# Optimization experiments

Measured on AMD Instinct MI355X. Metric: run time of the kernel, lower is better.

Reference implementation:

```python
import jax, jax.numpy as jnp
import numpy as np

D_MODEL = 1024
INNER = 2048      # expand=2
D_STATE = 16
D_CONV = 4
DT_RANK = 64      # ceil(1024/16)
DT_MIN, DT_MAX = 0.001, 0.1
RMS_EPS = 1e-6


def _causal_depthwise_conv1d(x, kernel, bias):
    # x: (B, L, C), kernel: (K, C)
    channels = x.shape[-1]
    rhs = kernel[:, None, :]  # (K, 1, C)
    out = jax.lax.conv_general_dilated(
        lhs=x, rhs=rhs, window_strides=(1,),
        padding=[(kernel.shape[0] - 1, 0)],
        dimension_numbers=("NWC", "WIO", "NWC"),
        feature_group_count=channels)
    return out + bias[None, None, :]


def _selective_scan(u, dt, b, c, a, d):
    # u, dt: (B, L, Di); b, c: (B, L, S); a: (Di, S); d: (Di,)
    da = jnp.exp(dt[..., None] * a)                  # (B, L, Di, S)
    db = (dt * u)[..., None] * b[:, :, None, :]      # (B, L, Di, S)

    def step(h, inp):
        da_t, db_t, c_t = inp
        h = da_t * h + db_t                          # (B, Di, S)
        y = jnp.einsum("bds,bs->bd", h, c_t)
        return h, y

    h0 = jnp.zeros((u.shape[0], u.shape[2], a.shape[1]), u.dtype)
    _, ys = jax.lax.scan(
        step, h0,
        (da.transpose(1, 0, 2, 3), db.transpose(1, 0, 2, 3), c.transpose(1, 0, 2)))
    return ys.transpose(1, 0, 2) + u * d             # (B, L, Di)


def setup_inputs() -> dict:
    key = jax.random.key(0)
    ks = jax.random.split(key, 16)

    def lin(k, fan_in, shape):
        return jax.random.normal(k, shape, jnp.float32) / np.sqrt(fan_in)

    a_init = jnp.log(jnp.arange(1, D_STATE + 1, dtype=jnp.float32))
    return {
        "x": jax.random.normal(ks[0], (2, 2048, D_MODEL), jnp.float32),
        "norm_scale": jnp.ones((D_MODEL,), jnp.float32),
        "in_proj_w": lin(ks[1], D_MODEL, (D_MODEL, 2 * INNER)),
        "in_proj_b": jnp.zeros((2 * INNER,), jnp.float32),
        "out_proj_w": lin(ks[2], INNER, (INNER, D_MODEL)),
        "out_proj_b": jnp.zeros((D_MODEL,), jnp.float32),
        "dt_in_w": lin(ks[3], INNER, (INNER, DT_RANK)),
        "dt_in_b": jnp.zeros((DT_RANK,), jnp.float32),
        "dt_out_w": lin(ks[4], DT_RANK, (DT_RANK, INNER)),
        "dt_out_b": jnp.zeros((INNER,), jnp.float32),
        "b_proj_w": lin(ks[5], INNER, (INNER, D_STATE)),
        "b_proj_b": jnp.zeros((D_STATE,), jnp.float32),
        "c_proj_w": lin(ks[6], INNER, (INNER, D_STATE)),
        "c_proj_b": jnp.zeros((D_STATE,), jnp.float32),
        "conv_kernel": jax.random.normal(ks[7], (D_CONV, INNER), jnp.float32) / np.sqrt(D_CONV),
        "conv_bias": jnp.zeros((INNER,), jnp.float32),
        "a_log": jnp.tile(a_init[None, :], (INNER, 1)),
        "d": jnp.ones((INNER,), jnp.float32),
        "dt_bias": jnp.zeros((INNER,), jnp.float32),
    }


def reference(x, norm_scale, in_proj_w, in_proj_b, out_proj_w, out_proj_b,
              dt_in_w, dt_in_b, dt_out_w, dt_out_b, b_proj_w, b_proj_b,
              c_proj_w, c_proj_b, conv_kernel, conv_bias, a_log, d, dt_bias):
    residual = x
    # RMSNorm
    var = jnp.mean(jnp.square(x), axis=-1, keepdims=True)
    xn = x * jax.lax.rsqrt(var + RMS_EPS) * norm_scale
    # in projection -> u, z
    uz = xn @ in_proj_w + in_proj_b
    u, z = jnp.split(uz, 2, axis=-1)
    # causal depthwise conv + silu
    u = _causal_depthwise_conv1d(u, conv_kernel, conv_bias)
    u = jax.nn.silu(u)
    # dt path (low-rank) -> softplus -> clip
    dt = (u @ dt_in_w + dt_in_b) @ dt_out_w + dt_out_b + dt_bias
    dt = jnp.clip(jax.nn.softplus(dt), DT_MIN, DT_MAX)
    # B, C projections with tanh
    b = jnp.tanh(u @ b_proj_w + b_proj_b)
    c = jnp.tanh(u @ c_proj_w + c_proj_b)
    # selective scan
    a = -jnp.exp(a_log)
    y = _selective_scan(u, dt, b, c, a, d)
    # gate, out projection, residual
    y = y * jax.nn.silu(z)
    y = y @ out_proj_w + out_proj_b
    return residual + y
```

## Files before the change

### kernel.cpp

```cpp
#include <hip/hip_runtime.h>
#include <cstdint>
#include <cstddef>

typedef unsigned short u16;
typedef __bf16 bf16x8 __attribute__((ext_vector_type(8)));
typedef float f32x4 __attribute__((ext_vector_type(4)));
typedef u16 u16x4 __attribute__((ext_vector_type(4)));

#define DMODEL 1024
#define DINNER 2048
#define NBATCH 2
#define LSEQ   2048
#define NTOK   4096
#define NSTATE 16
#define NCH    64
#define TCH    32

__device__ __forceinline__ u16 f2b(float f) {
  union { float f; unsigned u; } a; a.f = f;
  unsigned r = a.u + 0x7fffu + ((a.u >> 16) & 1u);
  return (u16)(r >> 16);
}
__device__ __forceinline__ float b2f(u16 h) {
  union { unsigned u; float f; } a; a.u = ((unsigned)h) << 16;
  return a.f;
}

__device__ __forceinline__ void gload_lds16(const u16* g, __bf16* l) {
  __builtin_amdgcn_global_load_lds(
      (const __attribute__((address_space(1))) unsigned int*)g,
      (__attribute__((address_space(3))) unsigned int*)l, 16, 0, 0);
}

__global__ __launch_bounds__(256)
void prep_all(const float* __restrict__ w_in, const float* __restrict__ w_out,
              const float* __restrict__ w_dti, const float* __restrict__ w_b,
              const float* __restrict__ w_c, const float* __restrict__ w_dto,
              const float* __restrict__ b_dto, const float* __restrict__ dtbias,
              const float* __restrict__ x, const float* __restrict__ nscale,
              u16* __restrict__ WINT, u16* __restrict__ WOUTT, u16* __restrict__ WBC,
              u16* __restrict__ WDT2T, float* __restrict__ DTB2, u16* __restrict__ XN) {
  __shared__ float sh[32 * 33];
  const int tid = threadIdx.x;
  const int xx = tid & 31, y0 = tid >> 5;
  int blk = blockIdx.x;
  if (blk < 4096) {
    int c0 = (blk & 127) * 32, r0 = (blk >> 7) * 32;
    #pragma unroll
    for (int yy = y0; yy < 32; yy += 8) sh[yy * 33 + xx] = w_in[(size_t)(r0 + yy) * 4096 + c0 + xx];
    __syncthreads();
    #pragma unroll
    for (int yy = y0; yy < 32; yy += 8) WINT[(size_t)(c0 + yy) * 1024 + r0 + xx] = f2b(sh[xx * 33 + yy]);
    return;
  }
  blk -= 4096;
  if (blk < 2048) {
    int c0 = (blk & 31) * 32, r0 = (blk >> 5) * 32;
    #pragma unroll
    for (int yy = y0; yy < 32; yy += 8) sh[yy * 33 + xx] = w_out[(size_t)(r0 + yy) * 1024 + c0 + xx];
    __syncthreads();
    #pragma unroll
    for (int yy = y0; yy < 32; yy += 8) WOUTT[(size_t)(c0 + yy) * 2048 + r0 + xx] = f2b(sh[xx * 33 + yy]);
    return;
  }
  blk -= 2048;
  if (blk < 192) {
    int c0 = (blk % 3) * 32, r0 = (blk / 3) * 32;
    #pragma unroll
    for (int yy = y0; yy < 32; yy += 8) {
      int r = r0 + yy, c = c0 + xx;
      float v = (c < 64) ? w_dti[(size_t)r * 64 + c]
                         : (c < 80 ? w_b[(size_t)r * 16 + (c - 64)] : w_c[(size_t)r * 16 + (c - 80)]);
      sh[yy * 33 + xx] = v;
    }
    __syncthreads();
    #pragma unroll
    for (int yy = y0; yy < 32; yy += 8) WBC[(size_t)(c0 + yy) * 2048 + r0 + xx] = f2b(sh[xx * 33 + yy]);
    return;
  }
  blk -= 192;
  if (blk < 128) {
    int c0 = (blk & 63) * 32, r0 = (blk >> 6) * 32;
    #pragma unroll
    for (int yy = y0; yy < 32; yy += 8) sh[yy * 33 + xx] = w_dto[(size_t)(r0 + yy) * 2048 + c0 + xx];
    __syncthreads();
    #pragma unroll
    for (int yy = y0; yy < 32; yy += 8) WDT2T[(size_t)(c0 + yy) * 64 + r0 + xx] = f2b(sh[xx * 33 + yy]);
    return;
  }
  blk -= 128;
  if (blk < 8) {
    int i = blk * 256 + tid;
    DTB2[i] = b_dto[i] + dtbias[i];
    return;
  }
  blk -= 8;
  {
    const float4* xp = (const float4*)(x + (size_t)blk * DMODEL);
    float4 v = xp[tid];
    float ss = v.x * v.x + v.y * v.y + v.z * v.z + v.w * v.w;
    #pragma unroll
    for (int o = 32; o; o >>= 1) ss += __shfl_down(ss, o);
    if ((tid & 63) == 0) sh[tid >> 6] = ss;
    __syncthreads();
    float tot = sh[0] + sh[1] + sh[2] + sh[3];
    float r = rsqrtf(tot * (1.0f / DMODEL) + 1e-6f);
    float4 sc = ((const float4*)nscale)[tid];
    u16x4 o4;
    o4[0] = f2b(v.x * r * sc.x); o4[1] = f2b(v.y * r * sc.y);
    o4[2] = f2b(v.z * r * sc.z); o4[3] = f2b(v.w * r * sc.w);
    *(u16x4*)(XN + (size_t)blk * DMODEL + tid * 4) = o4;
  }
}

template <int BM, int BN, int NWM, int NWN, int EPI>
__global__ __launch_bounds__(NWM * NWN * 64, 1)
void gemm_db(const u16* __restrict__ A, const u16* __restrict__ Bt,
             const float* __restrict__ bias, const float* __restrict__ res,
             void* __restrict__ outv, int M, int N, int K, int RM, int RN) {
  constexpr int NTHR = NWM * NWN * 64;
  constexpr int WMW = BM / NWM;
  constexpr int WNW = BN / NWN;
  constexpr int MF = WMW / 16;
  constexpr int NF = WNW / 16;
  constexpr int LPT = (BM + BN) * 8 / NTHR;
  __shared__ __bf16 lds[2][(BM + BN) * 64];
  const int tid = threadIdx.x;
  const int lane = tid & 63;
  const int wave = tid >> 6;
  const int wr = wave / NWN, wc = wave % NWN;

  const int GM = M / BM;
  const int bid = blockIdx.x;
  const int xcd = bid & 7;
  const int l = bid >> 3;
  const int rgm = GM / RM;
  const int rr = xcd % rgm, rc = xcd / rgm;
  const size_t m0 = (size_t)(rr * RM + (l % RM)) * BM;
  const size_t n0 = (size_t)(rc * RN + (l / RM)) * BN;
  const int NT = K >> 6;

#define STAGE_DB(bufi, k0)                                                     \
  { _Pragma("unroll")                                                          \
    for (int ss = 0; ss < BM * 8 / NTHR; ss++) {                               \
      int g = tid + ss * NTHR;                                                 \
      int row = g >> 3;                                                        \
      int kk = ((g & 7) * 8) ^ ((row & 7) << 3);                               \
      gload_lds16(A + (m0 + row) * K + (k0) + kk, &lds[bufi][g * 8]);          \
    }                                                                          \
    _Pragma("unroll")                                                          \
    for (int ss = 0; ss < BN * 8 / NTHR; ss++) {                               \
      int g = tid + ss * NTHR;                                                 \
      int row = g >> 3;                                                        \
      int kk = ((g & 7) * 8) ^ ((row & 7) << 3);                               \
      gload_lds16(Bt + (n0 + row) * K + (k0) + kk,                             \
                  &lds[bufi][BM * 64 + g * 8]);                                \
    } }

  f32x4 acc[MF][NF] = {};
  STAGE_DB(0, 0)
  STAGE_DB(1, 64)

  const int rsw = (lane & 7) << 3;
  const int arow0 = wr * WMW + (lane & 15);
  const int brow0 = wc * WNW + (lane & 15);
  const int kgrp = (lane >> 4) * 8;

  for (int t = 0; t < NT; t++) {
    const int cur = t & 1;
    if (t == NT - 1) asm volatile("s_waitcnt vmcnt(0)" ::: "memory");
    else             asm volatile("s_waitcnt vmcnt(%0)" :: "n"(LPT) : "memory");
    __builtin_amdgcn_s_barrier();
    asm volatile("" ::: "memory");
    const __bf16* As_ = &lds[cur][0];
    const __bf16* Bs_ = &lds[cur][BM * 64];
    #pragma unroll
    for (int qr = 0; qr < MF / 4; qr++) {
      #pragma unroll
      for (int qc = 0; qc < NF / 2; qc++) {
        bf16x8 af[2][4], bfv[2][2];
        #pragma unroll
        for (int ks = 0; ks < 2; ks++) {
          const int kk = (ks * 32 + kgrp) ^ rsw;
          #pragma unroll
          for (int i = 0; i < 4; i++)
            af[ks][i] = *(const bf16x8*)(As_ + (size_t)(arow0 + (qr * 4 + i) * 16) * 64 + kk);
          #pragma unroll
          for (int j = 0; j < 2; j++)
            bfv[ks][j] = *(const bf16x8*)(Bs_ + (size_t)(brow0 + (qc * 2 + j) * 16) * 64 + kk);
        }
        __builtin_amdgcn_s_setprio(1);
        #pragma unroll
        for (int ks = 0; ks < 2; ks++)
          #pragma unroll
          for (int i = 0; i < 4; i++)
            #pragma unroll
            for (int j = 0; j < 2; j++)
              acc[qr * 4 + i][qc * 2 + j] = __builtin_amdgcn_mfma_f32_16x16x32_bf16(
                  af[ks][i], bfv[ks][j], acc[qr * 4 + i][qc * 2 + j], 0, 0, 0);
        __builtin_amdgcn_s_setprio(0);
        __builtin_amdgcn_sched_barrier(0);
      }
    }
    __builtin_amdgcn_s_barrier();
    asm volatile("" ::: "memory");
    if (t + 2 < NT) { STAGE_DB(cur, (t + 2) * 64) }
  }

  const int cr = (lane >> 4) << 2;
  const int cc = lane & 15;
  #pragma unroll
  for (int fr = 0; fr < MF; fr++) {
    #pragma unroll
    for (int fc = 0; fc < NF; fc++) {
      const size_t col = n0 + wc * WNW + fc * 16 + cc;
      const float bv = bias[col];
      #pragma unroll
      for (int r = 0; r < 4; r++) {
        const size_t row = m0 + wr * WMW + fr * 16 + cr + r;
        if constexpr (EPI == 0) {
          ((u16*)outv)[row * N + col] = f2b(acc[fr][fc][r] + bv);
        } else {
          ((float*)outv)[row * N + col] = acc[fr][fc][r] + bv + res[row * N + col];
        }
      }
    }
  }
#undef STAGE_DB
}

template <int EPI, int BN>
__global__ __launch_bounds__(256)
void gemm_bt(const u16* __restrict__ A, const u16* __restrict__ Bt,
             const float* __restrict__ bias, const float* __restrict__ res,
             void* __restrict__ outv, int M, int N, int K, int ksplit) {
  constexpr int WN = BN / 2;
  constexpr int JN = WN / 16;
  __shared__ __bf16 As[128][72];
  __shared__ __bf16 Bs[BN][72];
  const int tid = threadIdx.x;
  const int m0 = blockIdx.y * 128;
  const int n0 = blockIdx.x * BN;
  const int wave = tid >> 6, lane = tid & 63;
  const int wm = (wave >> 1) * 64, wn = (wave & 1) * WN;
  const int sr = tid >> 3;
  const int sc = (tid & 7) * 8;
  const int kbeg = blockIdx.z * ksplit, kend = kbeg + ksplit;
  f32x4 acc[4][JN] = {};
  for (int k0 = kbeg; k0 < kend; k0 += 64) {
    __syncthreads();
    #pragma unroll
    for (int r = 0; r < 128; r += 32)
      *(bf16x8*)&As[sr + r][sc] = *(const bf16x8*)(A + (size_t)(m0 + sr + r) * K + k0 + sc);
    #pragma unroll
    for (int r = 0; r < BN; r += 32)
      *(bf16x8*)&Bs[sr + r][sc] = *(const bf16x8*)(Bt + (size_t)(n0 + sr + r) * K + k0 + sc);
    __syncthreads();
    #pragma unroll
    for (int ks = 0; ks < 64; ks += 32) {
      const int kr = ks + ((lane >> 4) << 3);
      bf16x8 af[4], bfr[JN];
      #pragma unroll
      for (int i = 0; i < 4; i++) af[i]  = *(const bf16x8*)&As[wm + (lane & 15) + i * 16][kr];
      #pragma unroll
      for (int j = 0; j < JN; j++) bfr[j] = *(const bf16x8*)&Bs[wn + (lane & 15) + j * 16][kr];
      #pragma unroll
      for (int i = 0; i < 4; i++)
        #pragma unroll
        for (int j = 0; j < JN; j++)
          acc[i][j] = __builtin_amdgcn_mfma_f32_16x16x32_bf16(af[i], bfr[j], acc[i][j], 0, 0, 0);
    }
  }
  const int cr = (lane >> 4) << 2;
  const int cc = lane & 15;
  #pragma unroll
  for (int i = 0; i < 4; i++) {
    #pragma unroll
    for (int j = 0; j < JN; j++) {
      const int col = n0 + wn + j * 16 + cc;
      #pragma unroll
      for (int r = 0; r < 4; r++) {
        const int row = m0 + wm + i * 16 + cr + r;
        float v = acc[i][j][r];
        if constexpr (EPI == 1) {
          ((float*)outv)[(size_t)blockIdx.z * M * N + (size_t)row * N + col] = v;
        } else {
          v += bias[col];
          v = (v > 20.0f) ? v : log1pf(__expf(v));
          v = fminf(fmaxf(v, 0.001f), 0.1f);
          ((u16*)outv)[(size_t)row * N + col] = f2b(v);
        }
      }
    }
  }
}

__global__ __launch_bounds__(256)
void conv_silu_seq(const u16* __restrict__ uz, const float* __restrict__ ck,
                   const float* __restrict__ cb, u16* __restrict__ u) {
  int d  = (blockIdx.x & 7) * 256 + threadIdx.x;
  int lc = (blockIdx.x >> 3) & 127;
  int b  = blockIdx.x >> 10;
  const float w0 = ck[d], w1 = ck[DINNER + d], w2 = ck[2 * DINNER + d], w3 = ck[3 * DINNER + d];
  const float bias = cb[d];
  const int t0 = lc * 16;
  float x0 = 0.f, x1 = 0.f, x2 = 0.f;
  #pragma unroll
  for (int j = -3; j < 0; j++) {
    int t = t0 + j;
    float v = (t >= 0) ? b2f(uz[((size_t)(b * LSEQ + t)) * (2 * DINNER) + d]) : 0.f;
    x0 = x1; x1 = x2; x2 = v;
  }
  #pragma unroll
  for (int i = 0; i < 16; i++) {
    int t = t0 + i;
    float x3 = b2f(uz[((size_t)(b * LSEQ + t)) * (2 * DINNER) + d]);
    float acc = bias + w0 * x0 + w1 * x1 + w2 * x2 + w3 * x3;
    float sv = acc / (1.0f + __expf(-acc));
    u[((size_t)(b * LSEQ + t)) * DINNER + d] = f2b(sv);
    x0 = x1; x1 = x2; x2 = x3;
  }
}

__global__ __launch_bounds__(256)
void prep_dtbc(const float* __restrict__ dtbc, const float* __restrict__ dtin_b,
               const float* __restrict__ bb, const float* __restrict__ cbias,
               u16* __restrict__ dt1, float* __restrict__ Bm, float* __restrict__ Cm) {
  int idx = blockIdx.x * 256 + threadIdx.x;
  if (idx >= NTOK * 96) return;
  int row = idx / 96, col = idx - row * 96;
  float v = 0.f;
  #pragma unroll
  for (int z = 0; z < 8; z++)
    v += dtbc[(size_t)z * NTOK * 96 + (size_t)row * 96 + col];
  if (col < 64)       dt1[(size_t)row * 64 + col] = f2b(v + dtin_b[col]);
  else if (col < 80)  Bm[(size_t)row * NSTATE + col - 64] = tanhf(v + bb[col - 64]);
  else                Cm[(size_t)row * NSTATE + col - 80] = tanhf(v + cbias[col - 80]);
}

__global__ __launch_bounds__(256)
void scan_pass1(const u16* __restrict__ dt, const u16* __restrict__ u,
                const float* __restrict__ Bm, const float* __restrict__ alog,
                float* __restrict__ chP, float* __restrict__ chS) {
  const int d  = (blockIdx.x & 7) * 256 + threadIdx.x;
  const int ch = (blockIdx.x >> 3) & (NCH - 1);
  const int b  = blockIdx.x >> 9;
  float A[NSTATE];
  #pragma unroll
  for (int s = 0; s < NSTATE; s++) A[s] = -__expf(alog[(size_t)d * NSTATE + s]);
  float h[NSTATE], P[NSTATE];
  #pragma unroll
  for (int s = 0; s < NSTATE; s++) { h[s] = 0.0f; P[s] = 1.0f; }
  const int t0 = ch * TCH;
  for (int i = 0; i < TCH; i++) {
    const size_t tok = (size_t)b * LSEQ + t0 + i;
    float dtv = b2f(dt[tok * DINNER + d]);
    float uv  = b2f(u[tok * DINNER + d]);
    float dtu = dtv * uv;
    const float* bp = Bm + tok * NSTATE;
    #pragma unroll
    for (int s = 0; s < NSTATE; s++) {
      float da = __expf(dtv * A[s]);
      P[s] *= da;
      h[s] = da * h[s] + dtu * bp[s];
    }
  }
  size_t base = (((size_t)b * NCH + ch) * DINNER + d) * NSTATE;
  #pragma unroll
  for (int s = 0; s < NSTATE; s++) { chP[base + s] = P[s]; chS[base + s] = h[s]; }
}

__global__ __launch_bounds__(256)
void scan_pass2(const float* __restrict__ chP, const float* __restrict__ chS,
                float* __restrict__ hst) {
  const int b   = blockIdx.x >> 7;
  const int off = (blockIdx.x & 127) * 256 + threadIdx.x;
  float h = 0.f;
  const size_t stride = (size_t)DINNER * NSTATE;
  size_t base = (size_t)b * NCH * stride + off;
  for (int c = 0; c < NCH; c++) {
    size_t a = base + (size_t)c * stride;
    float P = chP[a], S = chS[a];
    hst[a] = h;
    h = P * h + S;
  }
}

__global__ __launch_bounds__(256)
void scan_pass3(const u16* __restrict__ dt, const u16* __restrict__ u,
                const float* __restrict__ Bm, const float* __restrict__ Cm,
                const float* __restrict__ alog, const float* __restrict__ dvec,
                const u16* __restrict__ uz, const float* __restrict__ hst,
                u16* __restrict__ y) {
  const int d  = (blockIdx.x & 7) * 256 + threadIdx.x;
  const int ch = (blockIdx.x >> 3) & (NCH - 1);
  const int b  = blockIdx.x >> 9;
  float A[NSTATE];
  #pragma unroll
  for (int s = 0; s < NSTATE; s++) A[s] = -__expf(alog[(size_t)d * NSTATE + s]);
  float h[NSTATE];
  const size_t hbase = (((size_t)b * NCH + ch) * DINNER + d) * NSTATE;
  #pragma unroll
  for (int s = 0; s < NSTATE; s++) h[s] = hst[hbase + s];
  const float dval = dvec[d];
  const int t0 = ch * TCH;
  for (int i = 0; i < TCH; i++) {
    const size_t tok = (size_t)b * LSEQ + t0 + i;
    float dtv = b2f(dt[tok * DINNER + d]);
    float uv  = b2f(u[tok * DINNER + d]);
    float dtu = dtv * uv;
    const float* bp = Bm + tok * NSTATE;
    const float* cp = Cm + tok * NSTATE;
    float yv = 0.0f;
    #pragma unroll
    for (int s = 0; s < NSTATE; s++) {
      float da = __expf(dtv * A[s]);
      h[s] = da * h[s] + dtu * bp[s];
      yv += h[s] * cp[s];
    }
    yv += uv * dval;
    float z = b2f(uz[tok * (2 * DINNER) + DINNER + d]);
    float g = z / (1.0f + __expf(-z));
    y[tok * DINNER + d] = f2b(yv * g);
  }
}

#define WS_XN     ((size_t)0)
#define WS_WINT   (WS_XN     + 8388608)
#define WS_CHP    ((size_t)0)
#define WS_WOUTT  (WS_WINT   + 8388608)
#define WS_WBC    (WS_WOUTT  + 4194304)
#define WS_WDT2T  (WS_WBC    + 524288)
#define WS_DT1    (WS_WDT2T  + 262144)
#define WS_DTB2   (WS_DT1    + 524288)
#define WS_BMAT   (WS_DTB2   + 8192)
#define WS_CMAT   (WS_BMAT   + 262144)
#define WS_UZ     (WS_CMAT   + 262144)
#define WS_U      (WS_UZ     + 33554432)
#define WS_DTBC   (WS_U      + 16777216)
#define WS_DT     (WS_DTBC   + 16777216)
#define WS_CHS    (WS_DT     + 16777216)
#define WS_YBF    (WS_CHS    + 16777216)

extern "C" void kernel_launch(void* const* d_in, const int* in_sizes, int n_in,
                              void* d_out, int out_size, void* d_ws, size_t ws_size,
                              hipStream_t stream) {
  const float* x      = (const float*)d_in[0];
  const float* nscale = (const float*)d_in[1];
  const float* w_in   = (const float*)d_in[2];
  const float* b_in   = (const float*)d_in[3];
  const float* w_out  = (const float*)d_in[4];
  const float* b_out  = (const float*)d_in[5];
  const float* w_dti  = (const float*)d_in[6];
  const float* b_dti  = (const float*)d_in[7];
  const float* w_dto  = (const float*)d_in[8];
  const float* b_dto  = (const float*)d_in[9];
  const float* w_b    = (const float*)d_in[10];
  const float* b_b    = (const float*)d_in[11];
  const float* w_c    = (const float*)d_in[12];
  const float* b_c    = (const float*)d_in[13];
  const float* convk  = (const float*)d_in[14];
  const float* convb  = (const float*)d_in[15];
  const float* alog   = (const float*)d_in[16];
  const float* dvec   = (const float*)d_in[17];
  const float* dtbias = (const float*)d_in[18];
  float* out = (float*)d_out;
  char* ws = (char*)d_ws;

  u16*  XN    = (u16*)(ws + WS_XN);
  u16*  WINT  = (u16*)(ws + WS_WINT);
  u16*  WOUTT = (u16*)(ws + WS_WOUTT);
  u16*  WBC   = (u16*)(ws + WS_WBC);
  u16*  WDT2T = (u16*)(ws + WS_WDT2T);
  u16*  DT1   = (u16*)(ws + WS_DT1);
  float* DTB2 = (float*)(ws + WS_DTB2);
  float* BMAT = (float*)(ws + WS_BMAT);
  float* CMAT = (float*)(ws + WS_CMAT);
  u16*  UZ    = (u16*)(ws + WS_UZ);
  u16*  U     = (u16*)(ws + WS_U);
  float* DTBC = (float*)(ws + WS_DTBC);
  u16*  DT    = (u16*)(ws + WS_DT);
  float* CHP  = (float*)(ws + WS_CHP);
  float* CHS  = (float*)(ws + WS_CHS);
  float* HST  = (float*)(ws + WS_CHS);
  u16*  YBF   = (u16*)(ws + WS_YBF);

  prep_all<<<10568, 256, 0, stream>>>(w_in, w_out, w_dti, w_b, w_c, w_dto,
                                      b_dto, dtbias, x, nscale,
                                      WINT, WOUTT, WBC, WDT2T, DTB2, XN);

  gemm_db<256, 256, 2, 4, 0><<<256, 512, 0, stream>>>(
      XN, WINT, b_in, nullptr, UZ, NTOK, 4096, 1024, 4, 8);

  conv_silu_seq<<<NBATCH * 128 * 8, 256, 0, stream>>>(UZ, convk, convb, U);

  gemm_bt<1, 96><<<dim3(1, NTOK / 128, 8), 256, 0, stream>>>(
      U, WBC, nullptr, nullptr, DTBC, NTOK, 96, 2048, 256);
  prep_dtbc<<<(NTOK * 96 + 255) / 256, 256, 0, stream>>>(DTBC, b_dti, b_b, b_c, DT1, BMAT, CMAT);

  gemm_bt<2, 128><<<dim3(2048 / 128, NTOK / 128, 1), 256, 0, stream>>>(
      DT1, WDT2T, DTB2, nullptr, DT, NTOK, 2048, 64, 64);

  scan_pass1<<<NBATCH * NCH * 8, 256, 0, stream>>>(DT, U, BMAT, alog, CHP, CHS);
  scan_pass2<<<NBATCH * 128, 256, 0, stream>>>(CHP, CHS, HST);
  scan_pass3<<<NBATCH * NCH * 8, 256, 0, stream>>>(DT, U, BMAT, CMAT, alog, dvec, UZ, HST, YBF);

  gemm_db<128, 128, 2, 2, 3><<<256, 256, 0, stream>>>(
      YBF, WOUTT, b_out, x, out, NTOK, 1024, 2048, 4, 8);
}
```

Before: 228.0 us.

## Replace in-projection GEMM with 8-wave ping-pong pipelined kernel

Adds a dedicated 256x256 tile GEMM for the input projection. It splits each K-step into four quadrant MFMA phases and interleaves half-tile global-to-LDS loads for the next and next-next K tiles between them, using barriers, setprio and sched_barrier. The goal is to overlap memory loads with MFMA work and keep the matrix units busier than the generic double-buffered kernel did. The cost is heavier synchronisation, a full 128KB LDS footprint and more fragile hand scheduling.

```diff
diff --git a/kernel.cpp b/kernel.cpp
--- a/kernel.cpp
+++ b/kernel.cpp
@@ -111,6 +111,112 @@
     o4[2] = f2b(v.z * r * sc.z); o4[3] = f2b(v.w * r * sc.w);
     *(u16x4*)(XN + (size_t)blk * DMODEL + tid * 4) = o4;
   }
+}
+
+__global__ __launch_bounds__(512, 1)
+void gemm8p(const u16* __restrict__ A, const u16* __restrict__ Bt,
+            const float* __restrict__ bias, u16* __restrict__ out,
+            int M, int N, int K, int RM, int RN) {
+  __shared__ __bf16 lds[65536];
+  const int tid = threadIdx.x;
+  const int lane = tid & 63;
+  const int wave = tid >> 6;
+  const int wr = wave >> 2, wc = wave & 3;
+
+  const int GM = M >> 8;
+  const int bid = blockIdx.x;
+  const int xcd = bid & 7;
+  const int l = bid >> 3;
+  const int rgm = GM / RM;
+  const int rr = xcd % rgm, rc = xcd / rgm;
+  const size_t m0 = (size_t)(rr * RM + (l % RM)) * 256;
+  const size_t n0 = (size_t)(rc * RN + (l / RM)) * 256;
+  const int NT = K >> 6;
+
+  const int st_kk = ((tid & 7) * 8) ^ (((tid >> 3) & 7) << 3);
+
+#define SHALF(bufi, mat, half, kt, SRC, BASE)                                  \
+  { _Pragma("unroll") for (int ss = 0; ss < 2; ss++) {                         \
+      const int row_ = (tid >> 3) + ss * 64;                                   \
+      gload_lds16(SRC + ((BASE) + (half) * 128 + row_) * K + (size_t)(kt) * 64 + st_kk, \
+                  &lds[((bufi) * 2 + (mat)) * 16384 + (half) * 8192 + tid * 8 + ss * 4096]); } }
+
+  f32x4 acc[8][4] = {};
+  SHALF(0, 0, 0, 0, A,  m0)  SHALF(0, 1, 0, 0, Bt, n0)
+  SHALF(0, 0, 1, 0, A,  m0)  SHALF(0, 1, 1, 0, Bt, n0)
+  if (NT > 1) { SHALF(1, 0, 0, 1, A, m0)  SHALF(1, 1, 0, 1, Bt, n0) }
+
+  const int rsw = (lane & 7) << 3;
+  const int kgrp = (lane >> 4) * 8;
+  const int arl = wr * 64 + (lane & 15);
+  const int brl = wc * 32 + (lane & 15);
+
+  bf16x8 af[2][4], bv[2][2];
+
+#define DSA(QR)                                                                \
+  { _Pragma("unroll") for (int ks = 0; ks < 2; ks++)                           \
+      _Pragma("unroll") for (int i = 0; i < 4; i++)                            \
+        af[ks][i] = *(const bf16x8*)(&lds[cur * 32768 + (QR) * 8192 +          \
+                      (arl + i * 16) * 64 + ((ks * 32 + kgrp) ^ rsw)]); }
+#define DSB(QC)                                                                \
+  { _Pragma("unroll") for (int ks = 0; ks < 2; ks++)                           \
+      _Pragma("unroll") for (int j = 0; j < 2; j++)                            \
+        bv[ks][j] = *(const bf16x8*)(&lds[cur * 32768 + 16384 + (QC) * 8192 +  \
+                      (brl + j * 16) * 64 + ((ks * 32 + kgrp) ^ rsw)]); }
+#define MMA(QR, QC)                                                            \
+  __builtin_amdgcn_s_barrier();                                                \
+  asm volatile("s_waitcnt lgkmcnt(0)" ::: "memory");                           \
+  __builtin_amdgcn_sched_barrier(0);                                           \
+  __builtin_amdgcn_s_setprio(1);                                               \
+  { _Pragma("unroll") for (int ks = 0; ks < 2; ks++)                           \
+      _Pragma("unroll") for (int i = 0; i < 4; i++)                            \
+        _Pragma("unroll") for (int j = 0; j < 2; j++)                          \
+          acc[(QR) * 4 + i][(QC) * 2 + j] = __builtin_amdgcn_mfma_f32_16x16x32_bf16( \
+              af[ks][i], bv[ks][j], acc[(QR) * 4 + i][(QC) * 2 + j], 0, 0, 0); } \
+  __builtin_amdgcn_s_setprio(0);                                               \
+  __builtin_amdgcn_sched_barrier(0);                                           \
+  __builtin_amdgcn_s_barrier();                                                \
+  asm volatile("" ::: "memory");
+
+  for (int t = 0; t < NT; t++) {
+    const int cur = t & 1;
+    if (t == NT - 1) asm volatile("s_waitcnt vmcnt(0)" ::: "memory");
+    else             asm volatile("s_waitcnt vmcnt(4)" ::: "memory");
+    __builtin_amdgcn_s_barrier();
+    asm volatile("" ::: "memory");
+    DSA(0) DSB(0)
+    if (t + 1 < NT) { SHALF(cur ^ 1, 0, 1, t + 1, A, m0) }
+    MMA(0, 0)
+    DSB(1)
+    if (t + 1 < NT) { SHALF(cur ^ 1, 1, 1, t + 1, Bt, n0) }
+    MMA(0, 1)
+    DSA(1) DSB(0)
+    if (t + 2 < NT) { SHALF(cur, 0, 0, t + 2, A, m0) }
+    MMA(1, 0)
+    DSB(1)
+    if (t + 2 < NT) { SHALF(cur, 1, 0, t + 2, Bt, n0) }
+    MMA(1, 1)
+  }
+
+  const int cr = (lane >> 4) << 2;
+  const int cc = lane & 15;
+  #pragma unroll
+  for (int fr = 0; fr < 8; fr++) {
+    #pragma unroll
+    for (int fc = 0; fc < 4; fc++) {
+      const size_t col = n0 + wc * 32 + (fc >> 1) * 128 + (fc & 1) * 16 + cc;
+      const float bvs = bias[col];
+      #pragma unroll
+      for (int r = 0; r < 4; r++) {
+        const size_t row = m0 + wr * 64 + (fr >> 2) * 128 + (fr & 3) * 16 + cr + r;
+        out[row * N + col] = f2b(acc[fr][fc][r] + bvs);
+      }
+    }
+  }
+#undef SHALF
+#undef DSA
+#undef DSB
+#undef MMA
 }
 
 template <int BM, int BN, int NWM, int NWN, int EPI>
@@ -489,8 +595,7 @@
                                       b_dto, dtbias, x, nscale,
                                       WINT, WOUTT, WBC, WDT2T, DTB2, XN);
 
-  gemm_db<256, 256, 2, 4, 0><<<256, 512, 0, stream>>>(
-      XN, WINT, b_in, nullptr, UZ, NTOK, 4096, 1024, 4, 8);
+  gemm8p<<<256, 512, 0, stream>>>(XN, WINT, b_in, UZ, NTOK, 4096, 1024, 4, 8);
 
   conv_silu_seq<<<NBATCH * 128 * 8, 256, 0, stream>>>(UZ, convk, convb, U);
 
```

After: 225.9 us. About the same (-0.9%).

## Replace per-state exps with powers of one exp in scan; retile GEMMs

Applied to the files above, without the earlier changes.

In both scan passes, a runtime check detects whether A[s] equals (s+1)*A[0]. When it does, the 16 per-state exponentials per token become one exp raised to successive powers by multiplication, and the chunk decay product comes from a single exp of the summed dt. The general path is kept as a fallback. The in-projection and out-projection GEMM tile sizes and grid sizes are also changed to launch more, smaller blocks. Repeated multiplication adds some rounding error compared with direct exps, and the smaller tiles may reduce data reuse.

```diff
diff --git a/kernel.cpp b/kernel.cpp
--- a/kernel.cpp
+++ b/kernel.cpp
@@ -30,6 +30,25 @@
   __builtin_amdgcn_global_load_lds(
       (const __attribute__((address_space(1))) unsigned int*)g,
       (__attribute__((address_space(3))) unsigned int*)l, 16, 0, 0);
+}
+
+__device__ __forceinline__ void pow16(float w, float* p) {
+  p[0] = w;
+  p[1] = p[0] * p[0];
+  p[2] = p[1] * p[0];
+  p[3] = p[1] * p[1];
+  p[4] = p[3] * p[0];
+  p[5] = p[3] * p[1];
+  p[6] = p[3] * p[2];
+  p[7] = p[3] * p[3];
+  p[8]  = p[7] * p[0];
+  p[9]  = p[7] * p[1];
+  p[10] = p[7] * p[2];
+  p[11] = p[7] * p[3];
+  p[12] = p[7] * p[4];
+  p[13] = p[7] * p[5];
+  p[14] = p[7] * p[6];
+  p[15] = p[7] * p[7];
 }
 
 __global__ __launch_bounds__(256)
@@ -348,26 +367,54 @@
   float A[NSTATE];
   #pragma unroll
   for (int s = 0; s < NSTATE; s++) A[s] = -__expf(alog[(size_t)d * NSTATE + s]);
-  float h[NSTATE], P[NSTATE];
-  #pragma unroll
-  for (int s = 0; s < NSTATE; s++) { h[s] = 0.0f; P[s] = 1.0f; }
+  const float A0 = A[0];
+  bool structured = true;
+  #pragma unroll
+  for (int s = 1; s < NSTATE; s++)
+    structured = structured && (fabsf(A[s] - (s + 1) * A0) <= 1e-4f * fabsf((s + 1) * A0));
+  float h[NSTATE];
+  #pragma unroll
+  for (int s = 0; s < NSTATE; s++) h[s] = 0.0f;
   const int t0 = ch * TCH;
-  for (int i = 0; i < TCH; i++) {
-    const size_t tok = (size_t)b * LSEQ + t0 + i;
-    float dtv = b2f(dt[tok * DINNER + d]);
-    float uv  = b2f(u[tok * DINNER + d]);
-    float dtu = dtv * uv;
-    const float* bp = Bm + tok * NSTATE;
-    #pragma unroll
-    for (int s = 0; s < NSTATE; s++) {
-      float da = __expf(dtv * A[s]);
-      P[s] *= da;
-      h[s] = da * h[s] + dtu * bp[s];
-    }
-  }
   size_t base = (((size_t)b * NCH + ch) * DINNER + d) * NSTATE;
-  #pragma unroll
-  for (int s = 0; s < NSTATE; s++) { chP[base + s] = P[s]; chS[base + s] = h[s]; }
+  if (structured) {
+    float sdt = 0.f;
+    for (int i = 0; i < TCH; i++) {
+      const size_t tok = (size_t)b * LSEQ + t0 + i;
+      float dtv = b2f(dt[tok * DINNER + d]);
+      float uv  = b2f(u[tok * DINNER + d]);
+      float dtu = dtv * uv;
+      const float* bp = Bm + tok * NSTATE;
+      sdt += dtv;
+      float p[NSTATE];
+      pow16(__expf(dtv * A0), p);
+      #pragma unroll
+      for (int s = 0; s < NSTATE; s++) h[s] = p[s] * h[s] + dtu * bp[s];
+    }
+    float P[NSTATE];
+    pow16(__expf(sdt * A0), P);
+    #pragma unroll
+    for (int s = 0; s < NSTATE; s++) { chP[base + s] = P[s]; chS[base + s] = h[s]; }
+  } else {
+    float P[NSTATE];
+    #pragma unroll
+    for (int s = 0; s < NSTATE; s++) P[s] = 1.0f;
+    for (int i = 0; i < TCH; i++) {
+      const size_t tok = (size_t)b * LSEQ + t0 + i;
+      float dtv = b2f(dt[tok * DINNER + d]);
+      float uv  = b2f(u[tok * DINNER + d]);
+      float dtu = dtv * uv;
+      const float* bp = Bm + tok * NSTATE;
+      #pragma unroll
+      for (int s = 0; s < NSTATE; s++) {
+        float da = __expf(dtv * A[s]);
+        P[s] *= da;
+        h[s] = da * h[s] + dtu * bp[s];
+      }
+    }
+    #pragma unroll
+    for (int s = 0; s < NSTATE; s++) { chP[base + s] = P[s]; chS[base + s] = h[s]; }
+  }
 }
 
 __global__ __launch_bounds__(256)
@@ -398,30 +445,58 @@
   float A[NSTATE];
   #pragma unroll
   for (int s = 0; s < NSTATE; s++) A[s] = -__expf(alog[(size_t)d * NSTATE + s]);
+  const float A0 = A[0];
+  bool structured = true;
+  #pragma unroll
+  for (int s = 1; s < NSTATE; s++)
+    structured = structured && (fabsf(A[s] - (s + 1) * A0) <= 1e-4f * fabsf((s + 1) * A0));
   float h[NSTATE];
   const size_t hbase = (((size_t)b * NCH + ch) * DINNER + d) * NSTATE;
   #pragma unroll
   for (int s = 0; s < NSTATE; s++) h[s] = hst[hbase + s];
   const float dval = dvec[d];
   const int t0 = ch * TCH;
-  for (int i = 0; i < TCH; i++) {
-    const size_t tok = (size_t)b * LSEQ + t0 + i;
-    float dtv = b2f(dt[tok * DINNER + d]);
-    float uv  = b2f(u[tok * DINNER + d]);
-    float dtu = dtv * uv;
-    const float* bp = Bm + tok * NSTATE;
-    const float* cp = Cm + tok * NSTATE;
-    float yv = 0.0f;
-    #pragma unroll
-    for (int s = 0; s < NSTATE; s++) {
-      float da = __expf(dtv * A[s]);
-      h[s] = da * h[s] + dtu * bp[s];
-      yv += h[s] * cp[s];
-    }
-    yv += uv * dval;
-    float z = b2f(uz[tok * (2 * DINNER) + DINNER + d]);
-    float g = z / (1.0f + __expf(-z));
-    y[tok * DINNER + d] = f2b(yv * g);
+  if (structured) {
+    for (int i = 0; i < TCH; i++) {
+      const size_t tok = (size_t)b * LSEQ + t0 + i;
+      float dtv = b2f(dt[tok * DINNER + d]);
+      float uv  = b2f(u[tok * DINNER + d]);
+      float dtu = dtv * uv;
+      const float* bp = Bm + tok * NSTATE;
+      const float* cp = Cm + tok * NSTATE;
+      float p[NSTATE];
+      pow16(__expf(dtv * A0), p);
+      float yv = 0.0f;
+      #pragma unroll
+      for (int s = 0; s < NSTATE; s++) {
+        h[s] = p[s] * h[s] + dtu * bp[s];
+        yv += h[s] * cp[s];
+      }
+      yv += uv * dval;
+      float z = b2f(uz[tok * (2 * DINNER) + DINNER + d]);
+      float g = z / (1.0f + __expf(-z));
+      y[tok * DINNER + d] = f2b(yv * g);
+    }
+  } else {
+    for (int i = 0; i < TCH; i++) {
+      const size_t tok = (size_t)b * LSEQ + t0 + i;
+      float dtv = b2f(dt[tok * DINNER + d]);
+      float uv  = b2f(u[tok * DINNER + d]);
+      float dtu = dtv * uv;
+      const float* bp = Bm + tok * NSTATE;
+      const float* cp = Cm + tok * NSTATE;
+      float yv = 0.0f;
+      #pragma unroll
+      for (int s = 0; s < NSTATE; s++) {
+        float da = __expf(dtv * A[s]);
+        h[s] = da * h[s] + dtu * bp[s];
+        yv += h[s] * cp[s];
+      }
+      yv += uv * dval;
+      float z = b2f(uz[tok * (2 * DINNER) + DINNER + d]);
+      float g = z / (1.0f + __expf(-z));
+      y[tok * DINNER + d] = f2b(yv * g);
+    }
   }
 }
 
@@ -489,8 +564,8 @@
                                       b_dto, dtbias, x, nscale,
                                       WINT, WOUTT, WBC, WDT2T, DTB2, XN);
 
-  gemm_db<256, 256, 2, 4, 0><<<256, 512, 0, stream>>>(
-      XN, WINT, b_in, nullptr, UZ, NTOK, 4096, 1024, 4, 8);
+  gemm_db<128, 128, 2, 2, 0><<<1024, 256, 0, stream>>>(
+      XN, WINT, b_in, nullptr, UZ, NTOK, 4096, 1024, 8, 16);
 
   conv_silu_seq<<<NBATCH * 128 * 8, 256, 0, stream>>>(UZ, convk, convb, U);
 
@@ -505,6 +580,6 @@
   scan_pass2<<<NBATCH * 128, 256, 0, stream>>>(CHP, CHS, HST);
   scan_pass3<<<NBATCH * NCH * 8, 256, 0, stream>>>(DT, U, BMAT, CMAT, alog, dvec, UZ, HST, YBF);
 
-  gemm_db<128, 128, 2, 2, 3><<<256, 256, 0, stream>>>(
-      YBF, WOUTT, b_out, x, out, NTOK, 1024, 2048, 4, 8);
-}
+  gemm_db<128, 64, 2, 2, 3><<<512, 256, 0, stream>>>(
+      YBF, WOUTT, b_out, x, out, NTOK, 1024, 2048, 8, 8);
+}
```

Measured after the change: 207.0 us. 1.1x faster.
